# Kernel tuning notes

Measured on AMD Instinct MI355X. Metric: run time of the kernel, lower is better.

Reference implementation:

```python
import jax, jax.numpy as jnp
import numpy as np


def dht(x):
    # torch.fft.fft defaults to the last dim; DHT-style real-imag combine
    X = jnp.fft.fft(x, axis=-1)
    return X.real - X.imag


def compl_mul3d(x, y):
    # Faithful port of the original (including flips over dims (0,1,2),
    # which are batch/channel/mode axes, and the real-valued idht output).
    Y = dht(y)  # real
    Xflip = jnp.roll(jnp.flip(x, axis=(0, 1, 2)), shift=(1, 1, 1), axis=(0, 1, 2))
    Yflip = jnp.roll(jnp.flip(y, axis=(0, 1, 2)), shift=(1, 1, 1), axis=(0, 1, 2))  # complex
    Yplus = 0.5 * (Y + Yflip)   # complex (real + complex promotes)
    Yminus = 0.5 * (Y - Yflip)
    Z = (jnp.einsum('bixyz,ioxyz->boxyz', x, Yplus)
         + jnp.einsum('bixyz,ioxyz->boxyz', Xflip, Yminus))
    n = int(np.prod(Z.shape))
    return dht(Z) / n  # real float32, matches torch idht


def setup_inputs() -> dict:
    key = jax.random.key(0)
    k1, k2 = jax.random.split(key)
    B, Ci, Co = 4, 32, 32
    S = 64
    M = 12
    scale = 1.0 / (Ci * Co)
    x = jax.random.normal(k1, (B, Ci, S, S, S), dtype=jnp.float32)
    # real/imag parts each uniform[0,1)*scale, matching torch.rand(cfloat)*scale
    weights = scale * jax.random.uniform(k2, (4, Ci, Co, M, M, M, 2), dtype=jnp.float32)
    return {"x": x, "weights": weights}


def reference(x, weights):
    m1, m2, m3 = weights.shape[3], weights.shape[4], weights.shape[5]
    w = (weights[..., 0] + 1j * weights[..., 1]).astype(jnp.complex64)  # [4,i,o,m1,m2,m3]
    B = x.shape[0]
    Co = w.shape[2]
    S1, S2, S3 = x.shape[2], x.shape[3], x.shape[4]

    x_ft = jnp.fft.rfftn(x, axes=(2, 3, 4))
    x_ft_mirror = jnp.fft.rfftn(jnp.flip(x, axis=(2, 3, 4)), axes=(2, 3, 4))
    x_ht = x_ft + x_ft_mirror  # [B,Ci,S1,S2,S3//2+1] complex64

    out_ht = jnp.zeros((B, Co, S1, S2, S3 // 2 + 1), dtype=jnp.complex64)
    z1 = compl_mul3d(x_ht[:, :, :m1, :m2, :m3], w[0])
    z2 = compl_mul3d(x_ht[:, :, -m1:, :m2, :m3], w[1])
    z3 = compl_mul3d(x_ht[:, :, :m1, -m2:, :m3], w[2])
    z4 = compl_mul3d(x_ht[:, :, -m1:, -m2:, :m3], w[3])
    out_ht = out_ht.at[:, :, :m1, :m2, :m3].set(z1.astype(jnp.complex64))
    out_ht = out_ht.at[:, :, -m1:, :m2, :m3].set(z2.astype(jnp.complex64))
    out_ht = out_ht.at[:, :, :m1, -m2:, :m3].set(z3.astype(jnp.complex64))
    out_ht = out_ht.at[:, :, -m1:, -m2:, :m3].set(z4.astype(jnp.complex64))

    return jnp.fft.irfftn(out_ht, s=(S1, S2, S3), axes=(2, 3, 4))
```

## Files before the change

kernel.cpp:

```cpp
#include <hip/hip_runtime.h>
#include <math.h>


#define OFF_ES   0
#define OFF_C12P 128
#define OFF_C12M 272
#define OFF_U2   512
#define SZ_U2    4718592
#define OFF_XHT  (OFF_U2 + SZ_U2)
#define SZ_XHT   1769472
#define OFF_YP   (OFF_XHT + SZ_XHT)
#define SZ_Y     3538944
#define OFF_YM   (OFF_YP + SZ_Y)
#define OFF_ZB   (OFF_YM + SZ_Y)
#define SZ_ZB    442368
#define OFF_ZZ   (OFF_ZB + SZ_ZB)
#define SZ_ZZ    884736
#define WS_FLOATS (OFF_ZZ + SZ_ZZ)

__global__ void k_init(float* __restrict__ ws) {
    int t = threadIdx.x;
    if (t < 64) {
        double th = 6.283185307179586476925286766559 * (double)t / 64.0;
        ws[OFF_ES + 2*t]     = (float)cos(th);
        ws[OFF_ES + 2*t + 1] = (float)sin(th);
    }
    if (t < 144) {
        int k = t / 12, z = t % 12;
        double th = 6.283185307179586476925286766559 * (double)((k*z) % 12) / 12.0;
        double c = cos(th), s = sin(th);
        ws[OFF_C12P + t] = (float)(c + s);
        ws[OFF_C12M + t] = (float)(s - c);
    }
}

__global__ __launch_bounds__(256) void k_p12(const float* __restrict__ x,
                                             float* __restrict__ ws) {
    __shared__ float xs[65 * 64];
    __shared__ float us[64 * 26];
    __shared__ float esh[128];
    int t = threadIdx.x;
    int blk = blockIdx.x;
    const float* xrow = x + (size_t)blk * 4096;
    if (t < 128) esh[t] = ws[OFF_ES + t];
#pragma unroll
    for (int j = 0; j < 16; ++j) {
        int idx = t + 256 * j;
        xs[65 * (idx >> 6) + (idx & 63)] = xrow[idx];
    }
    __syncthreads();
#pragma unroll
    for (int r = 0; r < 3; ++r) {
        int oidx = t + 256 * r;
        int a3 = oidx >> 6, n2 = oidx & 63;
        float ar = 0.f, ai = 0.f;
        int m = 0;
        const float* xr2 = &xs[65 * n2];
        for (int n3 = 0; n3 < 64; ++n3) {
            float c = esh[2*m], s = esh[2*m + 1];
            float v = xr2[n3];
            ar = fmaf(v, c, ar);
            ai = fmaf(-v, s, ai);
            m = (m + a3) & 63;
        }
        us[n2*26 + 2*a3] = ar; us[n2*26 + 2*a3 + 1] = ai;
    }
    __syncthreads();
    float* uo = ws + OFF_U2 + (size_t)blk * 576;
    for (int r = 0; r < 2; ++r) {
        int oidx = t + 256 * r;
        if (oidx >= 288) break;
        int a2 = oidx / 12, a3 = oidx - a2 * 12;
        int k2 = a2 < 12 ? a2 : a2 + 40;
        float ar = 0.f, ai = 0.f;
        int m = 0;
        for (int n2 = 0; n2 < 64; ++n2) {
            float c = esh[2*m], s = esh[2*m + 1];
            float ur = us[n2*26 + 2*a3], ui = us[n2*26 + 2*a3 + 1];
            ar += ur * c + ui * s;
            ai += ui * c - ur * s;
            m = (m + k2) & 63;
        }
        uo[2*oidx] = ar; uo[2*oidx + 1] = ai;
    }
}

__global__ __launch_bounds__(256) void k_p3(float* __restrict__ ws) {
    __shared__ float us[1536];
    __shared__ float esh[128];
    int t = threadIdx.x;
    int blk = blockIdx.x;
    int bi = blk / 24, a2 = blk - bi * 24;
    const float* u2 = ws + OFF_U2;
    for (int j = t; j < 1536; j += 256) {
        int n1 = j / 24, rem = j - n1 * 24;
        us[j] = u2[(size_t)(bi * 64 + n1) * 576 + a2 * 24 + rem];
    }
    if (t < 128) esh[t] = ws[OFF_ES + t];
    __syncthreads();
    int k2 = a2 < 12 ? a2 : a2 + 40;
    float* xo = ws + OFF_XHT;
    for (int r = 0; r < 2; ++r) {
        int oidx = t + 256 * r;
        if (oidx >= 288) break;
        int a1 = oidx / 12, a3 = oidx - a1 * 12;
        int k1 = a1 < 12 ? a1 : a1 + 40;
        float ar = 0.f, ai = 0.f;
        int m = 0;
        for (int n1 = 0; n1 < 64; ++n1) {
            float c = esh[2*m], s = esh[2*m + 1];
            float ur = us[n1*24 + 2*a3], ui = us[n1*24 + 2*a3 + 1];
            ar += ur * c + ui * s;
            ai += ui * c - ur * s;
            m = (m + k1) & 63;
        }
        int psi = (k1 + k2 + a3) & 63;
        float pc = esh[2*psi], ps = esh[2*psi + 1];
        float xr = ar + pc * ar + ps * ai;
        float xi = ai + ps * ar - pc * ai;
        size_t o = (((size_t)bi * 24 + a1) * 24 + a2) * 12 + a3;
        xo[2*o] = xr; xo[2*o + 1] = xi;
    }
}

__global__ __launch_bounds__(256) void k_w(const float* __restrict__ wts,
                                           float* __restrict__ ws, int q) {
    __shared__ float cp[144], cm[144];
    int t = threadIdx.x;
    if (t < 144) { cp[t] = ws[OFF_C12P + t]; cm[t] = ws[OFF_C12M + t]; }
    __syncthreads();
    int flat = blockIdx.x * 256 + t;
    int k  = flat % 12;
    int y  = (flat / 12) % 12;
    int xx = (flat / 144) % 12;
    int o  = (flat / 1728) % 32;
    int i  = flat / 55296;
    size_t wb = ((((size_t)q * 32 + i) * 32 + o) * 12 + xx) * 12 + y;
    const float* wrow = wts + wb * 24;
    float Y = 0.f;
#pragma unroll
    for (int z = 0; z < 12; ++z)
        Y += wrow[2*z] * cp[k*12 + z] + wrow[2*z + 1] * cm[k*12 + z];
    int fi = (32 - i) & 31, fo = (32 - o) & 31, fx = (xx == 0) ? 0 : 12 - xx;
    size_t fwb = (((((size_t)q * 32 + fi) * 32 + fo) * 12 + fx) * 12 + y) * 12 + k;
    float wfr = wts[2*fwb], wfi = wts[2*fwb + 1];
    float* yp = ws + OFF_YP;
    float* ym = ws + OFF_YM;
    yp[2*flat]     = 0.5f * (Y + wfr);
    yp[2*flat + 1] = 0.5f * wfi;
    ym[2*flat]     = 0.5f * (Y - wfr);
    ym[2*flat + 1] = -0.5f * wfi;
}

__global__ __launch_bounds__(256) void k_e1(float* __restrict__ ws, int q) {
    int t = threadIdx.x;
    int flat = blockIdx.x * 256 + t;
    int z  = flat % 12;
    int y  = (flat / 12) % 12;
    int xx = (flat / 144) % 12;
    int o  = (flat / 1728) % 32;
    int b  = flat / 55296;
    int o1 = (q & 1) ? 12 : 0, o2 = (q & 2) ? 12 : 0;
    const float* xht = ws + OFF_XHT;
    const float* yp  = ws + OFF_YP;
    const float* ym  = ws + OFF_YM;
    int fb = (4 - b) & 3;
    int fx = (xx == 0) ? 0 : 12 - xx;
    float zr = 0.f, zi = 0.f;
    for (int i = 0; i < 32; ++i) {
        int fi = (32 - i) & 31;
        size_t xidx  = (((size_t)(b * 32 + i) * 24 + (o1 + xx)) * 24 + (o2 + y)) * 12 + z;
        size_t fxidx = (((size_t)(fb * 32 + fi) * 24 + (o1 + fx)) * 24 + (o2 + y)) * 12 + z;
        size_t yidx  = ((((size_t)i * 32 + o) * 12 + xx) * 12 + y) * 12 + z;
        float xr = xht[2*xidx],  xi2 = xht[2*xidx + 1];
        float fr = xht[2*fxidx], fim = xht[2*fxidx + 1];
        float pr = yp[2*yidx], pi = yp[2*yidx + 1];
        float mr = ym[2*yidx], mi = ym[2*yidx + 1];
        zr += xr * pr - xi2 * pi + fr * mr - fim * mi;
        zi += xr * pi + xi2 * pr + fr * mi + fim * mr;
    }
    float* zb = ws + OFF_ZB;
    zb[2*flat] = zr; zb[2*flat + 1] = zi;
}

__global__ __launch_bounds__(256) void k_e2(float* __restrict__ ws, int q) {
    __shared__ float cp[144], cm[144];
    int t = threadIdx.x;
    if (t < 144) { cp[t] = ws[OFF_C12P + t]; cm[t] = ws[OFF_C12M + t]; }
    __syncthreads();
    int flat = blockIdx.x * 256 + t;
    int k  = flat % 12;
    int y  = (flat / 12) % 12;
    int xx = (flat / 144) % 12;
    int bo = flat / 1728;
    const float* row = ws + OFF_ZB + (size_t)(flat - k) * 2;
    float acc = 0.f;
#pragma unroll
    for (int z = 0; z < 12; ++z)
        acc += row[2*z] * cp[k*12 + z] + row[2*z + 1] * cm[k*12 + z];
    float scale = (k == 0 ? 1.f : 2.f) / 221184.f;
    int o1 = (q & 1) ? 12 : 0, o2 = (q & 2) ? 12 : 0;
    float* zz = ws + OFF_ZZ;
    zz[(((size_t)bo * 24 + (o1 + xx)) * 24 + (o2 + y)) * 12 + k] = acc * scale;
}

__global__ __launch_bounds__(256) void k_inv(const float* __restrict__ ws,
                                             float* __restrict__ out) {
    __shared__ float c1s[576];
    __shared__ float c2s[1536];
    __shared__ float esh[128];
    int t = threadIdx.x;
    int blk = blockIdx.x;
    int bo = blk >> 6, n1 = blk & 63;
    if (t < 128) esh[t] = ws[OFF_ES + t];
    __syncthreads();
    const float* zz = ws + OFF_ZZ + (size_t)bo * 6912;
    for (int r = 0; r < 2; ++r) {
        int e = t + 256 * r;
        if (e < 288) {
            float re = 0.f, im = 0.f;
#pragma unroll
            for (int a1 = 0; a1 < 24; ++a1) {
                float v = zz[a1 * 288 + e];
                int k1 = a1 < 12 ? a1 : a1 + 40;
                int m = (k1 * n1) & 63;
                re = fmaf(v, esh[2*m], re);
                im = fmaf(v, esh[2*m + 1], im);
            }
            c1s[2*e] = re; c1s[2*e + 1] = im;
        }
    }
    __syncthreads();
#pragma unroll
    for (int r = 0; r < 3; ++r) {
        int e = t + 256 * r;
        int n2 = e / 12, k3 = e - n2 * 12;
        float re = 0.f, im = 0.f;
#pragma unroll
        for (int a2 = 0; a2 < 24; ++a2) {
            float ur = c1s[a2*24 + 2*k3], ui = c1s[a2*24 + 2*k3 + 1];
            int k2 = a2 < 12 ? a2 : a2 + 40;
            int m = (k2 * n2) & 63;
            float c = esh[2*m], s = esh[2*m + 1];
            re += ur * c - ui * s;
            im += ur * s + ui * c;
        }
        c2s[2*e] = re; c2s[2*e + 1] = im;
    }
    float rc[12], rs[12];
    {
        int n3 = t & 63, m = 0;
#pragma unroll
        for (int k3 = 0; k3 < 12; ++k3) {
            rc[k3] = esh[2*m]; rs[k3] = esh[2*m + 1];
            m = (m + n3) & 63;
        }
    }
    __syncthreads();
    float* orow = out + (size_t)blk * 4096;
#pragma unroll
    for (int r = 0; r < 16; ++r) {
        int f = t + 256 * r;
        int n2 = f >> 6;
        const float* c2r = &c2s[n2 * 24];
        float acc = 0.f;
#pragma unroll
        for (int k3 = 0; k3 < 12; ++k3)
            acc += c2r[2*k3] * rc[k3] - c2r[2*k3 + 1] * rs[k3];
        orow[f] = acc * (1.f / 262144.f);
    }
}

extern "C" void kernel_launch(void* const* d_in, const int* in_sizes, int n_in,
                              void* d_out, int out_size, void* d_ws, size_t ws_size,
                              hipStream_t stream) {
    const float* x   = (const float*)d_in[0];
    const float* wts = (const float*)d_in[1];
    float* out = (float*)d_out;
    float* ws  = (float*)d_ws;
    if (ws_size < (size_t)WS_FLOATS * sizeof(float)) return;

    k_init<<<1, 256, 0, stream>>>(ws);
    k_p12<<<8192, 256, 0, stream>>>(x, ws);
    k_p3<<<3072, 256, 0, stream>>>(ws);
    for (int q = 0; q < 4; ++q) {
        k_w<<<6912, 256, 0, stream>>>(wts, ws, q);
        k_e1<<<864, 256, 0, stream>>>(ws, q);
        k_e2<<<864, 256, 0, stream>>>(ws, q);
    }
    k_inv<<<8192, 256, 0, stream>>>(ws, out);
}
```

Measured before the change: 563.1 us.

## Use even/odd symmetry and twiddle recurrences in forward partial DFT kernels

The first-axis DFT now exploits real-input symmetry, pairing x[n] with x[64-n] so that 31 even/odd terms replace 64 terms. Each thread keeps its row in registers and generates twiddles by complex-rotation recurrence instead of indexed shared-memory lookups. The second and third axis passes transpose their shared buffers so each thread reads contiguous float4 values and also use recurrence-generated twiddles. This cuts shared-memory traffic and work per output, at the cost of more register pressure and some accumulated rounding error from the recurrences.

```diff
diff --git a/kernel.cpp b/kernel.cpp
--- a/kernel.cpp
+++ b/kernel.cpp
@@ -36,90 +36,116 @@
 
 __global__ __launch_bounds__(256) void k_p12(const float* __restrict__ x,
                                              float* __restrict__ ws) {
-    __shared__ float xs[65 * 64];
-    __shared__ float us[64 * 26];
+    __shared__ __align__(16) float xs[64 * 66];
+    __shared__ __align__(16) float us[12 * 132];
     __shared__ float esh[128];
     int t = threadIdx.x;
+    int lane = t & 63, w = t >> 6;
     int blk = blockIdx.x;
     const float* xrow = x + (size_t)blk * 4096;
     if (t < 128) esh[t] = ws[OFF_ES + t];
 #pragma unroll
     for (int j = 0; j < 16; ++j) {
         int idx = t + 256 * j;
-        xs[65 * (idx >> 6) + (idx & 63)] = xrow[idx];
-    }
-    __syncthreads();
+        xs[(idx >> 6) * 66 + (idx & 63)] = xrow[idx];
+    }
+    __syncthreads();
+    float x0 = xs[lane * 66 + 0], x32 = xs[lane * 66 + 32];
+    float ev[31], od[31];
+#pragma unroll
+    for (int n = 1; n <= 31; ++n) {
+        float a = xs[lane * 66 + n], b = xs[lane * 66 + 64 - n];
+        ev[n - 1] = a + b;
+        od[n - 1] = a - b;
+    }
 #pragma unroll
     for (int r = 0; r < 3; ++r) {
-        int oidx = t + 256 * r;
-        int a3 = oidx >> 6, n2 = oidx & 63;
-        float ar = 0.f, ai = 0.f;
-        int m = 0;
-        const float* xr2 = &xs[65 * n2];
-        for (int n3 = 0; n3 < 64; ++n3) {
-            float c = esh[2*m], s = esh[2*m + 1];
-            float v = xr2[n3];
-            ar = fmaf(v, c, ar);
-            ai = fmaf(-v, s, ai);
-            m = (m + a3) & 63;
-        }
-        us[n2*26 + 2*a3] = ar; us[n2*26 + 2*a3 + 1] = ai;
+        int a3 = w + 4 * r;
+        float cd = esh[2 * a3], sd = esh[2 * a3 + 1];
+        float ar = x0 + ((a3 & 1) ? -x32 : x32);
+        float ai = 0.f;
+        float c = cd, s = sd;
+#pragma unroll
+        for (int n = 0; n < 31; ++n) {
+            ar = fmaf(ev[n], c, ar);
+            ai = fmaf(-od[n], s, ai);
+            float cn = fmaf(c, cd, -s * sd);
+            float sn = fmaf(c, sd,  s * cd);
+            c = cn; s = sn;
+        }
+        us[a3 * 132 + 2 * lane]     = ar;
+        us[a3 * 132 + 2 * lane + 1] = ai;
     }
     __syncthreads();
     float* uo = ws + OFF_U2 + (size_t)blk * 576;
-    for (int r = 0; r < 2; ++r) {
-        int oidx = t + 256 * r;
+    for (int rr = 0; rr < 2; ++rr) {
+        int oidx = t + 256 * rr;
         if (oidx >= 288) break;
         int a2 = oidx / 12, a3 = oidx - a2 * 12;
         int k2 = a2 < 12 ? a2 : a2 + 40;
+        float cd = esh[2 * k2], sd = esh[2 * k2 + 1];
+        const float* urow = &us[a3 * 132];
         float ar = 0.f, ai = 0.f;
-        int m = 0;
-        for (int n2 = 0; n2 < 64; ++n2) {
-            float c = esh[2*m], s = esh[2*m + 1];
-            float ur = us[n2*26 + 2*a3], ui = us[n2*26 + 2*a3 + 1];
-            ar += ur * c + ui * s;
-            ai += ui * c - ur * s;
-            m = (m + k2) & 63;
-        }
-        uo[2*oidx] = ar; uo[2*oidx + 1] = ai;
+        float c = 1.f, s = 0.f;
+#pragma unroll 8
+        for (int j = 0; j < 32; ++j) {
+            float4 uu = *(const float4*)&urow[4 * j];
+            ar += uu.x * c + uu.y * s;
+            ai += uu.y * c - uu.x * s;
+            float c1 = fmaf(c, cd, -s * sd);
+            float s1 = fmaf(c, sd,  s * cd);
+            ar += uu.z * c1 + uu.w * s1;
+            ai += uu.w * c1 - uu.z * s1;
+            c = fmaf(c1, cd, -s1 * sd);
+            s = fmaf(c1, sd,  s1 * cd);
+        }
+        uo[2 * oidx] = ar; uo[2 * oidx + 1] = ai;
     }
 }
 
 __global__ __launch_bounds__(256) void k_p3(float* __restrict__ ws) {
-    __shared__ float us[1536];
+    __shared__ __align__(16) float us3[12 * 132];
     __shared__ float esh[128];
     int t = threadIdx.x;
     int blk = blockIdx.x;
     int bi = blk / 24, a2 = blk - bi * 24;
     const float* u2 = ws + OFF_U2;
     for (int j = t; j < 1536; j += 256) {
-        int n1 = j / 24, rem = j - n1 * 24;
-        us[j] = u2[(size_t)(bi * 64 + n1) * 576 + a2 * 24 + rem];
+        int n1 = j / 24, q = j - n1 * 24;
+        float v = u2[(size_t)(bi * 64 + n1) * 576 + a2 * 24 + q];
+        us3[(q >> 1) * 132 + 2 * n1 + (q & 1)] = v;
     }
     if (t < 128) esh[t] = ws[OFF_ES + t];
     __syncthreads();
     int k2 = a2 < 12 ? a2 : a2 + 40;
     float* xo = ws + OFF_XHT;
-    for (int r = 0; r < 2; ++r) {
-        int oidx = t + 256 * r;
+    for (int rr = 0; rr < 2; ++rr) {
+        int oidx = t + 256 * rr;
         if (oidx >= 288) break;
         int a1 = oidx / 12, a3 = oidx - a1 * 12;
         int k1 = a1 < 12 ? a1 : a1 + 40;
+        float cd = esh[2 * k1], sd = esh[2 * k1 + 1];
+        const float* urow = &us3[a3 * 132];
         float ar = 0.f, ai = 0.f;
-        int m = 0;
-        for (int n1 = 0; n1 < 64; ++n1) {
-            float c = esh[2*m], s = esh[2*m + 1];
-            float ur = us[n1*24 + 2*a3], ui = us[n1*24 + 2*a3 + 1];
-            ar += ur * c + ui * s;
-            ai += ui * c - ur * s;
-            m = (m + k1) & 63;
+        float c = 1.f, s = 0.f;
+#pragma unroll 8
+        for (int j = 0; j < 32; ++j) {
+            float4 uu = *(const float4*)&urow[4 * j];
+            ar += uu.x * c + uu.y * s;
+            ai += uu.y * c - uu.x * s;
+            float c1 = fmaf(c, cd, -s * sd);
+            float s1 = fmaf(c, sd,  s * cd);
+            ar += uu.z * c1 + uu.w * s1;
+            ai += uu.w * c1 - uu.z * s1;
+            c = fmaf(c1, cd, -s1 * sd);
+            s = fmaf(c1, sd,  s1 * cd);
         }
         int psi = (k1 + k2 + a3) & 63;
-        float pc = esh[2*psi], ps = esh[2*psi + 1];
+        float pc = esh[2 * psi], ps = esh[2 * psi + 1];
         float xr = ar + pc * ar + ps * ai;
         float xi = ai + ps * ar - pc * ai;
         size_t o = (((size_t)bi * 24 + a1) * 24 + a2) * 12 + a3;
-        xo[2*o] = xr; xo[2*o + 1] = xi;
+        xo[2 * o] = xr; xo[2 * o + 1] = xi;
     }
 }
 
```

New measurement: 551.1 us. -2.1%, faster.
